# Kernel optimization log

Measured on AMD Instinct MI355X. Metric: run time of the kernel, lower is better.

## Reference

```python
import jax, jax.numpy as jnp
import numpy as np

IMG = 512
STRIDE = 16
K = 9
FM = IMG // STRIDE          # 32
N = FM * FM * K             # 9216 anchors
IOU_THR = 0.7
POST_NMS_TOPK = 300
C_FEAT = 512


def _conv(x, w, b, stride=1, padding='SAME'):
    y = jax.lax.conv_general_dilated(x, w, (stride, stride), padding,
                                     dimension_numbers=('NCHW', 'OIHW', 'NCHW'))
    return y + b[None, :, None, None]


def _make_anchors():
    scales = [64.0, 128.0, 256.0]
    ratios = [0.5, 1.0, 2.0]
    wh = np.array([[s * np.sqrt(r), s / np.sqrt(r)] for s in scales for r in ratios],
                  np.float32)                                    # [K,2]
    ctr = (np.arange(FM, dtype=np.float32) + 0.5) * STRIDE
    cy, cx = np.meshgrid(ctr, ctr, indexing='ij')               # [FM,FM]
    c = np.stack([cx, cy], -1)[:, :, None, :]                   # [FM,FM,1,2]
    half = wh[None, None, :, :] / 2.0                           # [1,1,K,2]
    boxes = np.concatenate([c - half, c + half], -1)            # [FM,FM,K,4]
    return boxes.reshape(-1, 4)


def setup_inputs():
    key = jax.random.key(0)
    ks = jax.random.split(key, 5)
    p = lambda k, shp, s: jax.random.normal(k, shp, jnp.float32) * s
    return {
        'input_image': jax.random.normal(ks[0], (1, 3, IMG, IMG), jnp.float32),
        'anchors': jnp.asarray(_make_anchors()),
        'w_bb': p(ks[1], (C_FEAT, 3, STRIDE, STRIDE), 0.05),
        'b_bb': jnp.zeros((C_FEAT,), jnp.float32),
        'w_rpn': p(ks[2], (C_FEAT, C_FEAT, 3, 3), 0.02),
        'b_rpn': jnp.zeros((C_FEAT,), jnp.float32),
        'w_cls': p(ks[3], (2 * K, C_FEAT, 1, 1), 0.01),
        'b_cls': jnp.zeros((2 * K,), jnp.float32),
        'w_box': p(ks[4], (4 * K, C_FEAT, 1, 1), 0.01),
        'b_box': jnp.zeros((4 * K,), jnp.float32),
    }


def _decode_clip(anchors, deltas):
    # apply_delta_to_anchors + clip_boxes
    wa = anchors[:, 2] - anchors[:, 0]
    ha = anchors[:, 3] - anchors[:, 1]
    cxa = anchors[:, 0] + 0.5 * wa
    cya = anchors[:, 1] + 0.5 * ha
    dx, dy = deltas[:, 0], deltas[:, 1]
    dw = jnp.clip(deltas[:, 2], -4.0, 4.0)   # numeric guard on exp
    dh = jnp.clip(deltas[:, 3], -4.0, 4.0)
    cx = cxa + dx * wa
    cy = cya + dy * ha
    w = wa * jnp.exp(dw)
    h = ha * jnp.exp(dh)
    x1 = jnp.maximum(cx - 0.5 * w, 0.0)
    y1 = jnp.maximum(cy - 0.5 * h, 0.0)
    x2 = jnp.minimum(cx + 0.5 * w, IMG - 1.0)
    y2 = jnp.minimum(cy + 0.5 * h, IMG - 1.0)
    return jnp.stack([x1, y1, x2, y2], -1)


def _iou_matrix(b):
    x1, y1, x2, y2 = b[:, 0], b[:, 1], b[:, 2], b[:, 3]
    area = (x2 - x1) * (y2 - y1)
    iw = jnp.clip(jnp.minimum(x2[:, None], x2[None, :]) - jnp.maximum(x1[:, None], x1[None, :]), 0.0)
    ih = jnp.clip(jnp.minimum(y2[:, None], y2[None, :]) - jnp.maximum(y1[:, None], y1[None, :]), 0.0)
    inter = iw * ih
    return inter / (area[:, None] + area[None, :] - inter + 1e-9)


def _nms_keep(boxes_sorted):
    # boxes_sorted: [N,4] in descending score order; greedy hard NMS.
    iou = jax.lax.stop_gradient(_iou_matrix(boxes_sorted))  # [N,N]
    idx = jnp.arange(N)

    def body(i, keep):
        sup = keep[i] & (iou[i] > IOU_THR) & (idx > i)
        return keep & ~sup

    return jax.lax.fori_loop(0, N, body, jnp.ones((N,), bool))


def reference(input_image, anchors, w_bb, b_bb, w_rpn, b_rpn, w_cls, b_cls, w_box, b_box):
    # backbone
    feat = jax.nn.relu(_conv(input_image, w_bb, b_bb, stride=STRIDE, padding='VALID'))  # [1,512,32,32]
    # rpn
    hid = jax.nn.relu(_conv(feat, w_rpn, b_rpn))
    cls = _conv(hid, w_cls, b_cls)   # [1,2K,FM,FM]
    box = _conv(hid, w_box, b_box)   # [1,4K,FM,FM]
    # foreground scores: cls_scores[:, k:, :, :]
    scores = cls[0, K:, :, :].transpose(1, 2, 0).reshape(-1)                    # [N]
    deltas = box[0].reshape(K, 4, FM, FM).transpose(2, 3, 0, 1).reshape(-1, 4)  # [N,4]
    proposals = _decode_clip(anchors, deltas)
    order = jnp.argsort(-scores)
    boxes_s = proposals[order]
    keep = _nms_keep(boxes_s)
    # first 300 kept boxes (score order); fixed shape via stable argsort on keep flag
    sel = jnp.argsort((~keep).astype(jnp.int32), stable=True)[:POST_NMS_TOPK]
    return boxes_s[sel]
```

## Files before the change

kernel.cpp:

```cpp
#include <hip/hip_runtime.h>
#include <stdint.h>

typedef unsigned long long u64;

#define PTOT 1024
#define CF   512
#define NBOX 9216
#define NPAD 9280
#define NW   144
#define TOPK 300
#define RCH  19

__device__ __forceinline__ uint32_t score_key(float s) {
  uint32_t b = __float_as_uint(s);
  uint32_t o = (b & 0x80000000u) ? ~b : (b | 0x80000000u);
  return ~o;
}

#define FMA16() do { \
  acc[0][0] = fmaf(bv.x, av.x, acc[0][0]); \
  acc[0][1] = fmaf(bv.x, av.y, acc[0][1]); \
  acc[0][2] = fmaf(bv.x, av.z, acc[0][2]); \
  acc[0][3] = fmaf(bv.x, av.w, acc[0][3]); \
  acc[1][0] = fmaf(bv.y, av.x, acc[1][0]); \
  acc[1][1] = fmaf(bv.y, av.y, acc[1][1]); \
  acc[1][2] = fmaf(bv.y, av.z, acc[1][2]); \
  acc[1][3] = fmaf(bv.y, av.w, acc[1][3]); \
  acc[2][0] = fmaf(bv.z, av.x, acc[2][0]); \
  acc[2][1] = fmaf(bv.z, av.y, acc[2][1]); \
  acc[2][2] = fmaf(bv.z, av.z, acc[2][2]); \
  acc[2][3] = fmaf(bv.z, av.w, acc[2][3]); \
  acc[3][0] = fmaf(bv.w, av.x, acc[3][0]); \
  acc[3][1] = fmaf(bv.w, av.y, acc[3][1]); \
  acc[3][2] = fmaf(bv.w, av.z, acc[3][2]); \
  acc[3][3] = fmaf(bv.w, av.w, acc[3][3]); \
} while (0)

__global__ __launch_bounds__(256) void k_wt(const float* __restrict__ w_rpn,
                                            const float* __restrict__ w_bb,
                                            float* __restrict__ wT,
                                            float* __restrict__ wT1) {
  __shared__ float T[32][33];
  int bx = blockIdx.x;
  const float* src; float* dst; int K, kb;
  if (bx < 144) { src = w_rpn; dst = wT; K = 4608; kb = bx * 32; }
  else          { src = w_bb;  dst = wT1; K = 768; kb = (bx - 144) * 32; }
  const int cob = blockIdx.y * 32;
  const int tx = threadIdx.x & 31, ty = threadIdx.x >> 5;
#pragma unroll
  for (int r = 0; r < 32; r += 8)
    T[ty + r][tx] = src[(cob + ty + r) * K + kb + tx];
  __syncthreads();
#pragma unroll
  for (int r = 0; r < 32; r += 8)
    dst[(kb + ty + r) * 512 + cob + tx] = T[tx][ty + r];
}

__global__ __launch_bounds__(256) void k_conv1(const float* __restrict__ img,
                                               const float* __restrict__ wT1,
                                               float* __restrict__ featP) {
  __shared__ __align__(16) float As[32][72];
  __shared__ __align__(16) float Bs[32][64];
  const int t = threadIdx.x;
  const int pbase = blockIdx.x * 64;
  const int cobase = blockIdx.y * 64;
  const int z = blockIdx.z;
  const int pg = t & 15, cg = t >> 4;
  const int pp0 = pg * 4, cc0 = cg * 4;
  const int py0 = pbase >> 5;
  float acc[4][4] = {};
  for (int kb = 0; kb < 256; kb += 32) {
    const int ky0 = kb >> 4;
#pragma unroll
    for (int l0 = 0; l0 < 2048; l0 += 256) {
      int l = l0 + t;
      int seg = l >> 9, off = l & 511;
      int py_off = seg >> 1, ky_off = seg & 1;
      int row = (py0 + py_off) * 16 + ky0 + ky_off;
      float v = img[(z * 512 + row) * 512 + off];
      As[ky_off * 16 + (off & 15)][py_off * 32 + (off >> 4)] = v;
    }
#pragma unroll
    for (int it = 0; it < 2; ++it) {
      int idx4 = it * 256 + t;
      int k = idx4 >> 4, co4 = (idx4 & 15) << 2;
      *(float4*)&Bs[k][co4] =
          *(const float4*)&wT1[(z * 256 + kb + k) * 512 + cobase + co4];
    }
    __syncthreads();
#pragma unroll
    for (int kk = 0; kk < 32; ++kk) {
      float4 av = *(const float4*)&As[kk][pp0];
      float4 bv = *(const float4*)&Bs[kk][cc0];
      FMA16();
    }
    __syncthreads();
  }
#pragma unroll
  for (int i = 0; i < 4; ++i) {
    float* o = &featP[((size_t)z * CF + cobase + cc0 + i) * PTOT + pbase + pp0];
    *(float4*)o = make_float4(acc[i][0], acc[i][1], acc[i][2], acc[i][3]);
  }
}

__global__ __launch_bounds__(256) void k_reduce1(const float* __restrict__ featP,
                                                 const float* __restrict__ bias,
                                                 float* __restrict__ feat) {
  int idx4 = blockIdx.x * 256 + threadIdx.x;
  int co = idx4 >> 8;
  const float4* f = (const float4*)featP;
  float4 a = f[idx4];
  float4 b = f[idx4 + 131072];
  float4 c = f[idx4 + 262144];
  float bb = bias[co];
  float4 o;
  o.x = fmaxf(a.x + b.x + c.x + bb, 0.f);
  o.y = fmaxf(a.y + b.y + c.y + bb, 0.f);
  o.z = fmaxf(a.z + b.z + c.z + bb, 0.f);
  o.w = fmaxf(a.w + b.w + c.w + bb, 0.f);
  ((float4*)feat)[idx4] = o;
}

__global__ __launch_bounds__(256) void k_conv2(const float* __restrict__ feat,
                                               const float* __restrict__ wT,
                                               float* __restrict__ hidP,
                                               int ciPerZ) {
  __shared__ __align__(16) float As[8][6][44];
  __shared__ __align__(16) float Bs[72 * 64];
  const int t = threadIdx.x;
  const int pyb = blockIdx.x * 4;
  const int cob = blockIdx.y * 64;
  const int z = blockIdx.z;
  const int cib = z * ciPerZ;
  const int pg = t & 15, cg = t >> 4;
  const int prow = pg >> 2, px0 = (pg & 3) * 8;
  const int co0 = cg * 4;
  float acc[4][8] = {};
  for (int cc = 0; cc < ciPerZ; cc += 8) {
    {
      int idx4 = t;
#pragma unroll
      for (int it = 0; it < 2; ++it, idx4 += 256) {
        if (idx4 < 480) {
          int ci = idx4 / 60;
          int rem = idx4 - ci * 60;
          int row = rem / 10;
          int col4 = (rem - row * 10) << 2;
          int x = col4 - 4;
          int gy = pyb + row - 1;
          float4 v = make_float4(0.f, 0.f, 0.f, 0.f);
          if (x >= 0 && x < 32 && gy >= 0 && gy < 32)
            v = *(const float4*)&feat[(cib + cc + ci) * PTOT + gy * 32 + x];
          *(float4*)&As[ci][row][col4] = v;
        }
      }
    }
    {
      const int kg0 = (cib + cc) * 9;
      int idx4 = t;
#pragma unroll
      for (int it = 0; it < 5; ++it, idx4 += 256) {
        if (idx4 < 1152) {
          int k = idx4 >> 4;
          int co4 = (idx4 & 15) << 2;
          *(float4*)&Bs[k * 64 + co4] =
              *(const float4*)&wT[(kg0 + k) * 512 + cob + co4];
        }
      }
    }
    __syncthreads();
#pragma unroll 1
    for (int ci = 0; ci < 8; ++ci) {
#pragma unroll
      for (int dy = 0; dy < 3; ++dy) {
        const float* Ar = &As[ci][prow + dy][px0];
        float rw[16];
        *(float4*)&rw[0]  = *(const float4*)&Ar[0];
        *(float4*)&rw[4]  = *(const float4*)&Ar[4];
        *(float4*)&rw[8]  = *(const float4*)&Ar[8];
        *(float4*)&rw[12] = *(const float4*)&Ar[12];
#pragma unroll
        for (int dx = 0; dx < 3; ++dx) {
          const float* Bp = &Bs[(ci * 9 + dy * 3 + dx) * 64 + co0];
          float4 b0 = *(const float4*)&Bp[0];
          float bm[4] = {b0.x, b0.y, b0.z, b0.w};
#pragma unroll
          for (int m = 0; m < 4; ++m)
#pragma unroll
            for (int j = 0; j < 8; ++j)
              acc[m][j] = fmaf(rw[3 + dx + j], bm[m], acc[m][j]);
        }
      }
    }
    __syncthreads();
  }
  const int prowg = pyb + prow;
#pragma unroll
  for (int m = 0; m < 4; ++m) {
    int co = cob + co0 + m;
    float* o = &hidP[((size_t)z * CF + co) * PTOT + prowg * 32 + px0];
    *(float4*)&o[0] = make_float4(acc[m][0], acc[m][1], acc[m][2], acc[m][3]);
    *(float4*)&o[4] = make_float4(acc[m][4], acc[m][5], acc[m][6], acc[m][7]);
  }
}

__global__ __launch_bounds__(256) void k_reduce2(const float* __restrict__ hidP,
                                                 const float* __restrict__ bias,
                                                 float* __restrict__ hid_t, int Z) {
  __shared__ float T[32][33];
  const int co0 = blockIdx.x * 32, p0 = blockIdx.y * 32;
  const int t = threadIdx.x;
  {
    int co = t >> 3, p4 = (t & 7) << 2;
    float4 s = make_float4(0.f, 0.f, 0.f, 0.f);
    for (int zz = 0; zz < Z; ++zz) {
      float4 v = *(const float4*)&hidP[((size_t)zz * CF + co0 + co) * PTOT + p0 + p4];
      s.x += v.x; s.y += v.y; s.z += v.z; s.w += v.w;
    }
    float b = bias[co0 + co];
    T[co][p4 + 0] = fmaxf(s.x + b, 0.f);
    T[co][p4 + 1] = fmaxf(s.y + b, 0.f);
    T[co][p4 + 2] = fmaxf(s.z + b, 0.f);
    T[co][p4 + 3] = fmaxf(s.w + b, 0.f);
  }
  __syncthreads();
  {
    int p = t >> 3, co4 = (t & 7) << 2;
    float4 o = make_float4(T[co4][p], T[co4 + 1][p], T[co4 + 2][p], T[co4 + 3][p]);
    *(float4*)&hid_t[(size_t)(p0 + p) * CF + co0 + co4] = o;
  }
}

__global__ __launch_bounds__(256) void k_heads(const float* __restrict__ hid_t,
                                               const float* __restrict__ wcls,
                                               const float* __restrict__ bcls,
                                               const float* __restrict__ wbox,
                                               const float* __restrict__ bbox,
                                               uint32_t* __restrict__ key32,
                                               float* __restrict__ deltas) {
  const int t = threadIdx.x;
  if (blockIdx.x == 256) {
    if (t < 64) key32[NBOX + t] = 0xFFFFFFFFu;
    return;
  }
  const int lane = t & 63, w = t >> 6;
  const int p = blockIdx.x * 4 + w;
  const float* hp = &hid_t[(size_t)p * CF + lane * 8];
  float4 h0 = *(const float4*)hp;
  float4 h1 = *(const float4*)(hp + 4);
#pragma unroll 1
  for (int ch = 0; ch < 45; ++ch) {
    const float* wp = (ch < 9) ? &wcls[(9 + ch) * CF] : &wbox[(ch - 9) * CF];
    float4 w0 = *(const float4*)(wp + lane * 8);
    float4 w1 = *(const float4*)(wp + lane * 8 + 4);
    float s = h0.x * w0.x + h0.y * w0.y + h0.z * w0.z + h0.w * w0.w +
              h1.x * w1.x + h1.y * w1.y + h1.z * w1.z + h1.w * w1.w;
#pragma unroll
    for (int off = 32; off >= 1; off >>= 1) s += __shfl_xor(s, off, 64);
    if (lane == 0) {
      if (ch < 9) key32[p * 9 + ch] = score_key(s + bcls[9 + ch]);
      else        deltas[p * 36 + (ch - 9)] = s + bbox[ch - 9];
    }
  }
}

__global__ __launch_bounds__(256) void k_rank(const uint32_t* __restrict__ key32,
                                              uint32_t* __restrict__ P) {
  const int t = threadIdx.x;
  const int lane = t & 63, w = t >> 6;
  const int a = blockIdx.x * 4 + w;
  if (a >= 145) return;
  const int by = blockIdx.y;
  const int ig = a * 64 + lane;
  const uint32_t ka = key32[ig];
  uint32_t cnt = 0;
#pragma unroll 1
  for (int w2 = 0; w2 < 8; ++w2) {
    int word = by * 8 + w2;
    if (word >= 145) break;
    const uint32_t* bk = &key32[word * 64];
    const int jbase = word * 64;
#pragma unroll
    for (int s = 0; s < 64; ++s) {
      uint32_t kb = bk[s];
      int j = jbase + s;
      cnt += (uint32_t)((kb < ka) || (kb == ka && j < ig));
    }
  }
  P[(size_t)by * NPAD + ig] = cnt;
}

__global__ __launch_bounds__(256) void k_rfin(const uint32_t* __restrict__ P,
                                              const float* __restrict__ anchors,
                                              const float* __restrict__ deltas,
                                              float4* __restrict__ boxesS) {
  int i = blockIdx.x * 256 + threadIdx.x;
  if (i >= NBOX) return;
  uint32_t rank = 0;
#pragma unroll
  for (int c = 0; c < RCH; ++c) rank += P[(size_t)c * NPAD + i];
  float4 a = ((const float4*)anchors)[i];
  float4 d = ((const float4*)deltas)[i];
  float wa = a.z - a.x, ha = a.w - a.y;
  float cxa = a.x + 0.5f * wa, cya = a.y + 0.5f * ha;
  float dw = fminf(fmaxf(d.z, -4.f), 4.f);
  float dh = fminf(fmaxf(d.w, -4.f), 4.f);
  float cx = cxa + d.x * wa, cy = cya + d.y * ha;
  float ww = wa * expf(dw), hh = ha * expf(dh);
  float x1 = fmaxf(cx - 0.5f * ww, 0.f);
  float y1 = fmaxf(cy - 0.5f * hh, 0.f);
  float x2 = fminf(cx + 0.5f * ww, 511.f);
  float y2 = fminf(cy + 0.5f * hh, 511.f);
  boxesS[rank] = make_float4(x1, y1, x2, y2);
}

__global__ __launch_bounds__(256) void k_iou(const float4* __restrict__ boxesS,
                                             u64* __restrict__ mask) {
  __shared__ float4 cb[4][64];
  __shared__ float ca[4][64];
  const int t = threadIdx.x;
  const int lane = t & 63, w = t >> 6;
  const int u = blockIdx.x;
  const int v = blockIdx.y * 4 + w + 1;
  int y = u + v; if (y >= 145) y -= 145;
  const int a_ = min(u, y), b_ = max(u, y);
  const int iw = a_, wj = b_ - 1;

  {
    float4 c = boxesS[wj * 64 + lane];
    cb[w][lane] = c;
    ca[w][lane] = (c.z - c.x) * (c.w - c.y);
  }
  __syncthreads();

  const int i = iw * 64 + lane;
  float4 a = boxesS[i];
  float areaA = (a.z - a.x) * (a.w - a.y);
  u64 bits = 0;
#pragma unroll 4
  for (int jj = 0; jj < 64; ++jj) {
    int j = wj * 64 + jj;
    float4 c = cb[w][jj];
    float iw_ = fmaxf(fminf(a.z, c.z) - fmaxf(a.x, c.x), 0.f);
    float ih_ = fmaxf(fminf(a.w, c.w) - fmaxf(a.y, c.y), 0.f);
    float inter = iw_ * ih_;
    float uni = areaA + ca[w][jj] - inter + 1e-9f;
    float thr = 0.7f * uni;
    bool pos = uni > 0.f;
    bool sup = pos && (inter > thr);
    if (pos && (fabsf(inter - thr) <= thr * 1e-5f))
      sup = (inter / uni) > 0.7f;
    bits |= ((u64)(sup && (j > i))) << jj;
  }
  mask[(size_t)i * NW + wj] = bits;
}

__global__ __launch_bounds__(64) void k_scan(const u64* __restrict__ mask,
                                             const float4* __restrict__ boxesS,
                                             float* __restrict__ out) {
  __shared__ u64 keepArr[NW];
  __shared__ int pf[NW + 2];
  __shared__ int outIdx[TOPK];
  const int lane = threadIdx.x;

  u64 r0 = 0, r1 = 0, r2 = 0;
  int keptCount = 0;
  int stopSpan = NW - 1;

  u64 dcur = mask[(size_t)lane * NW];

  for (int wb = 0; wb < NW; ++wb) {
    u64 v = (wb < 64) ? r0 : ((wb < 128) ? r1 : r2);
    u64 R = __shfl(v, wb & 63, 64);

    u64 dnext = 0;
    if (wb + 1 < NW)
      dnext = mask[(size_t)((wb + 1) * 64 + lane) * NW + (wb + 1)];

    u64 keepmask = 0;
    u64 notR = ~R;
    while (notR) {
      int rl = __ffsll((long long)notR) - 1;
      keepmask |= 1ull << rl;
      u64 drl = __shfl(dcur, rl, 64);
      R |= drl;
      u64 above = (rl >= 63) ? 0ull : (~0ull << (rl + 1));
      notR = ~R & above;
    }

    if (keepmask) {
      u64 km = keepmask;
      while (km) {
        int first = wb * 64 + __ffsll((long long)km) - 1;
        int idx[8];
#pragma unroll
        for (int s = 0; s < 8; ++s) {
          if (km) { idx[s] = wb * 64 + __ffsll((long long)km) - 1; km &= km - 1; }
          else    { idx[s] = first; }
        }
        u64 A[8], B[8], C[8];
#pragma unroll
        for (int s = 0; s < 8; ++s) {
          const u64* q = mask + (size_t)idx[s] * NW;
          A[s] = q[lane];
          B[s] = q[lane + 64];
          C[s] = (lane < 16) ? q[lane + 128] : 0ull;
        }
#pragma unroll
        for (int s = 0; s < 8; ++s) { r0 |= A[s]; r1 |= B[s]; r2 |= C[s]; }
      }
      keptCount += __popcll(keepmask);
    }
    if (lane == 0) keepArr[wb] = keepmask;
    dcur = dnext;
    if (keptCount >= TOPK) { stopSpan = wb; break; }
  }

  __syncthreads();
  if (lane == 0) {
    int acc = 0;
    for (int s = 0; s <= stopSpan; ++s) { pf[s] = acc; acc += __popcll(keepArr[s]); }
    pf[stopSpan + 1] = acc;
  }
  __syncthreads();
  const int keptTotal = pf[stopSpan + 1];

  for (int s = lane; s <= stopSpan; s += 64) {
    u64 km = keepArr[s];
    int slot = pf[s];
    while (km && slot < TOPK) {
      int rl = __ffsll((long long)km) - 1; km &= km - 1;
      outIdx[slot++] = s * 64 + rl;
    }
  }
  if (keptTotal < TOPK) {
    for (int s = lane; s <= stopSpan; s += 64) {
      u64 rm = ~keepArr[s];
      int slot = keptTotal + s * 64 - pf[s];
      while (rm && slot < TOPK) {
        int rl = __ffsll((long long)rm) - 1; rm &= rm - 1;
        outIdx[slot++] = s * 64 + rl;
      }
    }
  }
  __syncthreads();
#pragma unroll
  for (int k0 = 0; k0 < TOPK + 63; k0 += 64) {
    int k = k0 + lane;
    if (k < TOPK) {
      float4 bx = boxesS[outIdx[k]];
      out[k * 4 + 0] = bx.x;
      out[k * 4 + 1] = bx.y;
      out[k * 4 + 2] = bx.z;
      out[k * 4 + 3] = bx.w;
    }
  }
}

extern "C" void kernel_launch(void* const* d_in, const int* in_sizes, int n_in,
                              void* d_out, int out_size, void* d_ws, size_t ws_size,
                              hipStream_t stream) {
  const float* img   = (const float*)d_in[0];
  const float* anch  = (const float*)d_in[1];
  const float* w_bb  = (const float*)d_in[2];
  const float* b_bb  = (const float*)d_in[3];
  const float* w_rpn = (const float*)d_in[4];
  const float* b_rpn = (const float*)d_in[5];
  const float* w_cls = (const float*)d_in[6];
  const float* b_cls = (const float*)d_in[7];
  const float* w_box = (const float*)d_in[8];
  const float* b_box = (const float*)d_in[9];

  char* ws = (char*)d_ws;
  int Z = 16;
  if (ws_size < 22806528ull + 16ull * 2097152ull) Z = 8;
  if (ws_size < 22806528ull + 8ull * 2097152ull)  Z = 4;
  if (ws_size < 22806528ull + 4ull * 2097152ull)  Z = 2;
  if (ws_size < 22806528ull + 2ull * 2097152ull)  Z = 1;

  float* wT    = (float*)(ws);
  float* wT1   = (float*)(ws + 9437184);
  float* featP = (float*)(ws + 11010048);
  float* feat  = (float*)(ws + 17301504);
  float* hidP  = (float*)(ws + 19398656);
  char*  hte   = ws + 19398656 + (size_t)Z * 2097152;
  float* hid_t = (float*)hte;
  char*  tail  = hte + 2097152;
  float*    deltas = (float*)(tail);
  uint32_t* key32  = (uint32_t*)(tail + 0x28000);
  float4*   boxesS = (float4*)(tail + 0x38000);
  uint32_t* P      = (uint32_t*)(ws + 11010048);
  u64*      mask   = (u64*)(ws + 11010048);
  float*    out    = (float*)d_out;

  hipLaunchKernelGGL(k_wt, dim3(168, 16), dim3(256), 0, stream, w_rpn, w_bb, wT, wT1);
  hipLaunchKernelGGL(k_conv1, dim3(16, 8, 3), dim3(256), 0, stream, img, wT1, featP);
  hipLaunchKernelGGL(k_reduce1, dim3(512), dim3(256), 0, stream, featP, b_bb, feat);
  hipLaunchKernelGGL(k_conv2, dim3(8, 8, Z), dim3(256), 0, stream, feat, wT, hidP, 512 / Z);
  hipLaunchKernelGGL(k_reduce2, dim3(16, 32), dim3(256), 0, stream, hidP, b_rpn, hid_t, Z);
  hipLaunchKernelGGL(k_heads, dim3(257), dim3(256), 0, stream, hid_t, w_cls, b_cls, w_box, b_box, key32, deltas);
  hipLaunchKernelGGL(k_rank, dim3(37, RCH), dim3(256), 0, stream, key32, P);
  hipLaunchKernelGGL(k_rfin, dim3(37), dim3(256), 0, stream, P, anch, deltas, boxesS);
  hipLaunchKernelGGL(k_iou, dim3(145, 18), dim3(256), 0, stream, boxesS, mask);
  hipLaunchKernelGGL(k_scan, dim3(1), dim3(64), 0, stream, mask, boxesS, out);
}
```

Measured before the change: 307.3 us.

## Merge weight transpose and conv1 into one launch; fold reduce1 into conv2 loads

Combines the w_rpn transpose and the backbone conv into a single kernel, with block ranges picking the role. The conv now reads w_bb directly and transposes it while staging into shared memory, so the wT1 buffer is gone. The split-K partial sum, bias and ReLU from reduce1 are done inside conv2's input tile load. This removes two launches and a feature-map round trip, but conv2 now reads three partial buffers for every tile load, and that load is repeated across its co-blocks and z-splits.

After: 305.3 us, median of 2. Within noise of the previous version (-0.7%).

```diff
diff --git a/kernel.cpp b/kernel.cpp
--- a/kernel.cpp
+++ b/kernel.cpp
@@ -36,35 +36,35 @@
   acc[3][3] = fmaf(bv.w, av.w, acc[3][3]); \
 } while (0)
 
-__global__ __launch_bounds__(256) void k_wt(const float* __restrict__ w_rpn,
-                                            const float* __restrict__ w_bb,
-                                            float* __restrict__ wT,
-                                            float* __restrict__ wT1) {
-  __shared__ float T[32][33];
-  int bx = blockIdx.x;
-  const float* src; float* dst; int K, kb;
-  if (bx < 144) { src = w_rpn; dst = wT; K = 4608; kb = bx * 32; }
-  else          { src = w_bb;  dst = wT1; K = 768; kb = (bx - 144) * 32; }
-  const int cob = blockIdx.y * 32;
-  const int tx = threadIdx.x & 31, ty = threadIdx.x >> 5;
-#pragma unroll
-  for (int r = 0; r < 32; r += 8)
-    T[ty + r][tx] = src[(cob + ty + r) * K + kb + tx];
-  __syncthreads();
-#pragma unroll
-  for (int r = 0; r < 32; r += 8)
-    dst[(kb + ty + r) * 512 + cob + tx] = T[tx][ty + r];
-}
-
-__global__ __launch_bounds__(256) void k_conv1(const float* __restrict__ img,
-                                               const float* __restrict__ wT1,
+__global__ __launch_bounds__(256) void k_front(const float* __restrict__ w_rpn,
+                                               const float* __restrict__ w_bb,
+                                               const float* __restrict__ img,
+                                               float* __restrict__ wT,
                                                float* __restrict__ featP) {
   __shared__ __align__(16) float As[32][72];
   __shared__ __align__(16) float Bs[32][64];
-  const int t = threadIdx.x;
-  const int pbase = blockIdx.x * 64;
-  const int cobase = blockIdx.y * 64;
-  const int z = blockIdx.z;
+  __shared__ float Twt[32][33];
+  const int bid = blockIdx.x;
+  const int t = threadIdx.x;
+
+  if (bid < 2304) {
+    const int kb = (bid >> 4) * 32;
+    const int cob = (bid & 15) * 32;
+    const int tx = t & 31, ty = t >> 5;
+#pragma unroll
+    for (int r = 0; r < 32; r += 8)
+      Twt[ty + r][tx] = w_rpn[(cob + ty + r) * 4608 + kb + tx];
+    __syncthreads();
+#pragma unroll
+    for (int r = 0; r < 32; r += 8)
+      wT[(kb + ty + r) * 512 + cob + tx] = Twt[tx][ty + r];
+    return;
+  }
+
+  const int b2 = bid - 2304;
+  const int pbase = (b2 & 15) * 64;
+  const int cobase = ((b2 >> 4) & 7) * 64;
+  const int z = b2 >> 7;
   const int pg = t & 15, cg = t >> 4;
   const int pp0 = pg * 4, cc0 = cg * 4;
   const int py0 = pbase >> 5;
@@ -83,9 +83,13 @@
 #pragma unroll
     for (int it = 0; it < 2; ++it) {
       int idx4 = it * 256 + t;
-      int k = idx4 >> 4, co4 = (idx4 & 15) << 2;
-      *(float4*)&Bs[k][co4] =
-          *(const float4*)&wT1[(z * 256 + kb + k) * 512 + cobase + co4];
+      int co = idx4 & 63;
+      int k4 = (idx4 >> 6) * 4;
+      float4 v = *(const float4*)&w_bb[(size_t)(cobase + co) * 768 + z * 256 + kb + k4];
+      Bs[k4 + 0][co] = v.x;
+      Bs[k4 + 1][co] = v.y;
+      Bs[k4 + 2][co] = v.z;
+      Bs[k4 + 3][co] = v.w;
     }
     __syncthreads();
 #pragma unroll
@@ -103,25 +107,8 @@
   }
 }
 
-__global__ __launch_bounds__(256) void k_reduce1(const float* __restrict__ featP,
-                                                 const float* __restrict__ bias,
-                                                 float* __restrict__ feat) {
-  int idx4 = blockIdx.x * 256 + threadIdx.x;
-  int co = idx4 >> 8;
-  const float4* f = (const float4*)featP;
-  float4 a = f[idx4];
-  float4 b = f[idx4 + 131072];
-  float4 c = f[idx4 + 262144];
-  float bb = bias[co];
-  float4 o;
-  o.x = fmaxf(a.x + b.x + c.x + bb, 0.f);
-  o.y = fmaxf(a.y + b.y + c.y + bb, 0.f);
-  o.z = fmaxf(a.z + b.z + c.z + bb, 0.f);
-  o.w = fmaxf(a.w + b.w + c.w + bb, 0.f);
-  ((float4*)feat)[idx4] = o;
-}
-
-__global__ __launch_bounds__(256) void k_conv2(const float* __restrict__ feat,
+__global__ __launch_bounds__(256) void k_conv2(const float* __restrict__ featP,
+                                               const float* __restrict__ bias1,
                                                const float* __restrict__ wT,
                                                float* __restrict__ hidP,
                                                int ciPerZ) {
@@ -149,8 +136,18 @@
           int x = col4 - 4;
           int gy = pyb + row - 1;
           float4 v = make_float4(0.f, 0.f, 0.f, 0.f);
-          if (x >= 0 && x < 32 && gy >= 0 && gy < 32)
-            v = *(const float4*)&feat[(cib + cc + ci) * PTOT + gy * 32 + x];
+          if (x >= 0 && x < 32 && gy >= 0 && gy < 32) {
+            const int c = cib + cc + ci;
+            const float* f0 = &featP[(size_t)c * PTOT + gy * 32 + x];
+            float4 a0 = *(const float4*)f0;
+            float4 a1 = *(const float4*)(f0 + (size_t)CF * PTOT);
+            float4 a2 = *(const float4*)(f0 + (size_t)2 * CF * PTOT);
+            float b = bias1[c];
+            v.x = fmaxf(a0.x + a1.x + a2.x + b, 0.f);
+            v.y = fmaxf(a0.y + a1.y + a2.y + b, 0.f);
+            v.z = fmaxf(a0.z + a1.z + a2.z + b, 0.f);
+            v.w = fmaxf(a0.w + a1.w + a2.w + b, 0.f);
+          }
           *(float4*)&As[ci][row][col4] = v;
         }
       }
@@ -479,24 +476,20 @@
   if (ws_size < 22806528ull + 2ull * 2097152ull)  Z = 1;
 
   float* wT    = (float*)(ws);
-  float* wT1   = (float*)(ws + 9437184);
-  float* featP = (float*)(ws + 11010048);
-  float* feat  = (float*)(ws + 17301504);
-  float* hidP  = (float*)(ws + 19398656);
-  char*  hte   = ws + 19398656 + (size_t)Z * 2097152;
+  float* featP = (float*)(ws + 9437184);
+  float* hidP  = (float*)(ws + 15728640);
+  char*  hte   = ws + 15728640 + (size_t)Z * 2097152;
   float* hid_t = (float*)hte;
   char*  tail  = hte + 2097152;
   float*    deltas = (float*)(tail);
   uint32_t* key32  = (uint32_t*)(tail + 0x28000);
   float4*   boxesS = (float4*)(tail + 0x38000);
-  uint32_t* P      = (uint32_t*)(ws + 11010048);
-  u64*      mask   = (u64*)(ws + 11010048);
+  uint32_t* P      = (uint32_t*)(ws + 9437184);
+  u64*      mask   = (u64*)(ws);
   float*    out    = (float*)d_out;
 
-  hipLaunchKernelGGL(k_wt, dim3(168, 16), dim3(256), 0, stream, w_rpn, w_bb, wT, wT1);
-  hipLaunchKernelGGL(k_conv1, dim3(16, 8, 3), dim3(256), 0, stream, img, wT1, featP);
-  hipLaunchKernelGGL(k_reduce1, dim3(512), dim3(256), 0, stream, featP, b_bb, feat);
-  hipLaunchKernelGGL(k_conv2, dim3(8, 8, Z), dim3(256), 0, stream, feat, wT, hidP, 512 / Z);
+  hipLaunchKernelGGL(k_front, dim3(2688), dim3(256), 0, stream, w_rpn, w_bb, img, wT, featP);
+  hipLaunchKernelGGL(k_conv2, dim3(8, 8, Z), dim3(256), 0, stream, featP, b_bb, wT, hidP, 512 / Z);
   hipLaunchKernelGGL(k_reduce2, dim3(16, 32), dim3(256), 0, stream, hidP, b_rpn, hid_t, Z);
   hipLaunchKernelGGL(k_heads, dim3(257), dim3(256), 0, stream, hid_t, w_cls, b_cls, w_box, b_box, key32, deltas);
   hipLaunchKernelGGL(k_rank, dim3(37, RCH), dim3(256), 0, stream, key32, P);
```
